# Performance work log

Measured on AMD Instinct MI355X. Metric: run time of the kernel, lower is better.

Reference implementation:

```python
import jax, jax.numpy as jnp
import numpy as np
import math

EMBED_DIM = 512
NUM_HEADS = 8
BLOCK_SIZE = 16
RANK = 32
B, N = 1, 4096
HEAD_DIM = EMBED_DIM // NUM_HEADS
SCALE = math.sqrt(HEAD_DIM)  # note: the torch module MULTIPLIES q by sqrt(head_dim)


def _block_causal_mask(n, block):
    # block-diagonal lower-triangular mask, identical for every head
    idx = jnp.arange(n)
    same_block = (idx[:, None] // block) == (idx[None, :] // block)
    causal = idx[:, None] >= idx[None, :]
    return (same_block & causal).astype(jnp.float32)  # [N, N]


def setup_inputs() -> dict:
    key = jax.random.key(0)
    ks = jax.random.split(key, 12)
    s = 0.02
    C, R = EMBED_DIM, RANK
    return {
        "x": jax.random.normal(ks[0], (B, N, C), dtype=jnp.float32),
        # low-rank query proj: Linear(C->R) then Linear(R->C); torch weight is [out, in]
        "q_w1": jax.random.normal(ks[1], (R, C), dtype=jnp.float32) * s,
        "q_w2": jax.random.normal(ks[2], (C, R), dtype=jnp.float32) * s,
        # key_value: Linear(C->2R) then Linear(2R->2C)
        "kv_w1": jax.random.normal(ks[3], (2 * R, C), dtype=jnp.float32) * s,
        "kv_w2": jax.random.normal(ks[4], (2 * C, 2 * R), dtype=jnp.float32) * s,
        # dynamic_focus: depthwise 1x1 conv (per-channel scale+bias) then pointwise 1x1 conv
        "dw_w": jax.random.normal(ks[5], (C,), dtype=jnp.float32) * s,
        "dw_b": jax.random.normal(ks[6], (C,), dtype=jnp.float32) * s,
        "pw_w": jax.random.normal(ks[7], (C, C), dtype=jnp.float32) * s,
        "pw_b": jax.random.normal(ks[8], (C,), dtype=jnp.float32) * s,
        # output proj: Linear(C->R) then Linear(R->C)
        "p_w1": jax.random.normal(ks[9], (R, C), dtype=jnp.float32) * s,
        "p_w2": jax.random.normal(ks[10], (C, R), dtype=jnp.float32) * s,
    }


def reference(x, q_w1, q_w2, kv_w1, kv_w2, dw_w, dw_b, pw_w, pw_b, p_w1, p_w2):
    Bv, Nv, C = x.shape
    H, D = NUM_HEADS, HEAD_DIM

    # low-rank q / kv projections (no bias)
    q = (x @ q_w1.T) @ q_w2.T                              # [B, N, C]
    kv = (x @ kv_w1.T) @ kv_w2.T                           # [B, N, 2C]

    q = q.reshape(Bv, Nv, H, D).transpose(0, 2, 1, 3)      # [B, H, N, D]
    kv = kv.reshape(Bv, Nv, 2, H, D).transpose(2, 0, 3, 1, 4)
    k, v = kv[0], kv[1]                                    # [B, H, N, D]

    q = q * SCALE
    attn = jnp.einsum("bhnd,bhmd->bhnm", q, k)             # [B, H, N, N]
    # faithful to source: full-row softmax FIRST, then block-diag causal mask
    mask = _block_causal_mask(Nv, BLOCK_SIZE)              # [N, N]
    attn = jax.nn.softmax(attn, axis=-1) * mask

    wv = jnp.einsum("bhnm,bhmd->bhnd", attn, v)            # [B, H, N, D]
    wv = wv.transpose(0, 2, 1, 3).reshape(Bv, Nv, C)       # [B, N, C]

    # dynamic_focus: depthwise 1x1 conv == per-channel affine; pointwise 1x1 conv == linear.
    # Spatial reshape to (sqrt(N), sqrt(N)) is a no-op for 1x1 convs, so stay in [B, N, C].
    dyn = wv * dw_w + dw_b
    dyn = dyn @ pw_w.T + pw_b

    y = dyn + x
    y = (y @ p_w1.T) @ p_w2.T
    return y
```

## Files before the change

kernel.cpp:

```cpp
#include <hip/hip_runtime.h>

#define NFULL 4096
#define CDIM  512
#define HEADS 8
#define DDIM  64

typedef unsigned short u16;
typedef short bf16x8 __attribute__((ext_vector_type(8)));
typedef float f32x4 __attribute__((ext_vector_type(4)));

#if __has_builtin(__builtin_amdgcn_exp2f)
__device__ __forceinline__ float exp2_hw(float x) { return __builtin_amdgcn_exp2f(x); }
#else
__device__ __forceinline__ float exp2_hw(float x) {
  float r;
  asm volatile("v_exp_f32 %0, %1\n\ts_nop 1" : "=v"(r) : "v"(x));
  return r;
}
#endif
#define EXP2(x) exp2_hw(x)

#define QSCALE 11.541560327111707f

__device__ __forceinline__ float dot4(float4 a, float4 b) {
  return a.x * b.x + a.y * b.y + a.z * b.z + a.w * b.w;
}

__device__ __forceinline__ u16 f2bf(float x) {
  union { float f; unsigned u; } v; v.f = x;
  unsigned r = v.u + 0x7fffu + ((v.u >> 16) & 1u);
  return (u16)(r >> 16);
}

__global__ __launch_bounds__(256) void k_pre(const float* __restrict__ x,
                                             const float* __restrict__ qw1,
                                             const float* __restrict__ kvw1,
                                             float* __restrict__ t_part,
                                             const float* __restrict__ pww,
                                             const float* __restrict__ dww,
                                             const float* __restrict__ dwb,
                                             const float* __restrict__ pwb,
                                             float* __restrict__ bias2,
                                             u16* __restrict__ pwbf) {
  __shared__ __align__(16) u16 Xs[64][72];
  __shared__ __align__(16) u16 Ws[96][72];
  const int tid = threadIdx.x;
  if (blockIdx.x >= 128) {
    const int b = blockIdx.x - 128;
    if (b < 2) {
      const int c = b * 256 + tid;
      float acc = 0.f;
      for (int e = 0; e < 512; e += 4)
        acc += dot4(*(const float4*)&pww[(size_t)c * 512 + e], *(const float4*)&dwb[e]);
      bias2[c] = acc + pwb[c];
    } else {
      const int base = (b - 2) * 4096 + tid * 16;
      const int e0 = base & 511;
      u16 o[16];
#pragma unroll
      for (int q = 0; q < 4; ++q) {
        const float4 w = *(const float4*)&pww[base + q * 4];
        const float4 d = *(const float4*)&dww[e0 + q * 4];
        o[q * 4 + 0] = f2bf(w.x * d.x); o[q * 4 + 1] = f2bf(w.y * d.y);
        o[q * 4 + 2] = f2bf(w.z * d.z); o[q * 4 + 3] = f2bf(w.w * d.w);
      }
      *(uint4*)&pwbf[base] = *(const uint4*)&o[0];
      *(uint4*)&pwbf[base + 8] = *(const uint4*)&o[8];
    }
    return;
  }

  const int rb = blockIdx.x >> 1, ks = blockIdx.x & 1;
  const int r0 = rb * 64;
  const int wave = tid >> 6, lane = tid & 63;
  const int lrow = lane & 15, g = lane >> 4;

  f32x4 acc[6];
#pragma unroll
  for (int sub = 0; sub < 6; ++sub) acc[sub] = (f32x4){0.f, 0.f, 0.f, 0.f};

  for (int k0 = ks * 256; k0 < ks * 256 + 256; k0 += 64) {
    __syncthreads();
    {
      const int row = tid >> 2, c16 = (tid & 3) * 16;
      const float* __restrict__ src = x + (size_t)(r0 + row) * 512 + k0 + c16;
      u16 tmp[16];
#pragma unroll
      for (int q = 0; q < 4; ++q) {
        const float4 v = *(const float4*)(src + q * 4);
        tmp[q * 4 + 0] = f2bf(v.x); tmp[q * 4 + 1] = f2bf(v.y);
        tmp[q * 4 + 2] = f2bf(v.z); tmp[q * 4 + 3] = f2bf(v.w);
      }
      *(uint4*)&Xs[row][c16] = *(const uint4*)&tmp[0];
      *(uint4*)&Xs[row][c16 + 8] = *(const uint4*)&tmp[8];
    }
    for (int u = tid; u < 384; u += 256) {
      const int c = u >> 2, c16 = (u & 3) * 16;
      const float* __restrict__ src =
          (c < 32 ? qw1 + (size_t)c * 512 : kvw1 + (size_t)(c - 32) * 512) + k0 + c16;
      u16 tmp[16];
#pragma unroll
      for (int q = 0; q < 4; ++q) {
        const float4 v = *(const float4*)(src + q * 4);
        tmp[q * 4 + 0] = f2bf(v.x); tmp[q * 4 + 1] = f2bf(v.y);
        tmp[q * 4 + 2] = f2bf(v.z); tmp[q * 4 + 3] = f2bf(v.w);
      }
      *(uint4*)&Ws[c][c16] = *(const uint4*)&tmp[0];
      *(uint4*)&Ws[c][c16 + 8] = *(const uint4*)&tmp[8];
    }
    __syncthreads();
    const bf16x8 a0 = *(const bf16x8*)&Xs[wave * 16 + lrow][g * 8];
    const bf16x8 a1 = *(const bf16x8*)&Xs[wave * 16 + lrow][32 + g * 8];
#pragma unroll
    for (int sub = 0; sub < 6; ++sub) {
      const bf16x8 b0 = *(const bf16x8*)&Ws[sub * 16 + lrow][g * 8];
      const bf16x8 b1 = *(const bf16x8*)&Ws[sub * 16 + lrow][32 + g * 8];
      acc[sub] = __builtin_amdgcn_mfma_f32_16x16x32_bf16(a0, b0, acc[sub], 0, 0, 0);
      acc[sub] = __builtin_amdgcn_mfma_f32_16x16x32_bf16(a1, b1, acc[sub], 0, 0, 0);
    }
  }
  float* __restrict__ tp = t_part + (size_t)ks * NFULL * 96;
#pragma unroll
  for (int sub = 0; sub < 6; ++sub)
#pragma unroll
    for (int j = 0; j < 4; ++j)
      tp[(size_t)(r0 + wave * 16 + g * 4 + j) * 96 + sub * 16 + lrow] = acc[sub][j];
}

__global__ __launch_bounds__(256) void k_proj2(const float* __restrict__ t_part,
                                               const float* __restrict__ qw2,
                                               const float* __restrict__ kvw2,
                                               u16* __restrict__ qb,
                                               u16* __restrict__ kb,
                                               float* __restrict__ vh) {
  __shared__ __align__(16) u16 Ts[64][72];
  __shared__ __align__(16) u16 Wsh[128][72];
  const int cb = blockIdx.x % 12;
  const int r0 = (blockIdx.x / 12) * 64;
  const int tid = threadIdx.x;
  const int wave = tid >> 6, lane = tid & 63;
  const int lrow = lane & 15, g = lane >> 4;
  const bool isq = cb < 4;
  const int c0 = isq ? cb * 128 : 512 + (cb - 4) * 128;
  const float* __restrict__ tp0 = t_part;
  const float* __restrict__ tp1 = t_part + (size_t)NFULL * 96;

  if (isq) {
    for (int u = tid; u < 512; u += 256) {
      const int row = u >> 3, c4 = (u & 7) * 4;
      const size_t gi = (size_t)(r0 + row) * 96 + c4;
      const float4 p0 = *(const float4*)&tp0[gi];
      const float4 p1 = *(const float4*)&tp1[gi];
      u16 tmp[4] = {f2bf(p0.x + p1.x), f2bf(p0.y + p1.y),
                    f2bf(p0.z + p1.z), f2bf(p0.w + p1.w)};
      *(uint2*)&Ts[row][c4] = *(const uint2*)&tmp[0];
    }
  } else {
    for (int u = tid; u < 1024; u += 256) {
      const int row = u >> 4, c4 = (u & 15) * 4;
      const size_t gi = (size_t)(r0 + row) * 96 + 32 + c4;
      const float4 p0 = *(const float4*)&tp0[gi];
      const float4 p1 = *(const float4*)&tp1[gi];
      u16 tmp[4] = {f2bf(p0.x + p1.x), f2bf(p0.y + p1.y),
                    f2bf(p0.z + p1.z), f2bf(p0.w + p1.w)};
      *(uint2*)&Ts[row][c4] = *(const uint2*)&tmp[0];
    }
  }
  if (isq) {
    for (int u = tid; u < 1024; u += 256) {
      const int col = u >> 3, cf = (u & 7) * 4;
      const float4 v = *(const float4*)&qw2[(size_t)(c0 + col) * 32 + cf];
      u16 tmp[4] = {f2bf(v.x), f2bf(v.y), f2bf(v.z), f2bf(v.w)};
      *(uint2*)&Wsh[col][cf] = *(const uint2*)&tmp[0];
    }
  } else {
    for (int u = tid; u < 2048; u += 256) {
      const int col = u >> 4, cf = (u & 15) * 4;
      const float4 v = *(const float4*)&kvw2[(size_t)(c0 - 512 + col) * 64 + cf];
      u16 tmp[4] = {f2bf(v.x), f2bf(v.y), f2bf(v.z), f2bf(v.w)};
      *(uint2*)&Wsh[col][cf] = *(const uint2*)&tmp[0];
    }
  }
  __syncthreads();

  if (isq) {
    const bf16x8 aq = *(const bf16x8*)&Ts[wave * 16 + lrow][g * 8];
#pragma unroll
    for (int sub = 0; sub < 8; ++sub) {
      const bf16x8 b0 = *(const bf16x8*)&Wsh[sub * 16 + lrow][g * 8];
      f32x4 acc = {0.f, 0.f, 0.f, 0.f};
      acc = __builtin_amdgcn_mfma_f32_16x16x32_bf16(aq, b0, acc, 0, 0, 0);
      const int colg = c0 + sub * 16 + lrow;
#pragma unroll
      for (int j = 0; j < 4; ++j) {
        const int n = r0 + wave * 16 + g * 4 + j;
        qb[((size_t)(colg >> 6) * NFULL + n) * 64 + (colg & 63)] = f2bf(acc[j] * QSCALE);
      }
    }
  } else {
    const bf16x8 a0 = *(const bf16x8*)&Ts[wave * 16 + lrow][g * 8];
    const bf16x8 a1 = *(const bf16x8*)&Ts[wave * 16 + lrow][32 + g * 8];
#pragma unroll
    for (int sub = 0; sub < 8; ++sub) {
      const bf16x8 b0 = *(const bf16x8*)&Wsh[sub * 16 + lrow][g * 8];
      const bf16x8 b1 = *(const bf16x8*)&Wsh[sub * 16 + lrow][32 + g * 8];
      f32x4 acc = {0.f, 0.f, 0.f, 0.f};
      acc = __builtin_amdgcn_mfma_f32_16x16x32_bf16(a0, b0, acc, 0, 0, 0);
      acc = __builtin_amdgcn_mfma_f32_16x16x32_bf16(a1, b1, acc, 0, 0, 0);
      const int colg = c0 + sub * 16 + lrow;
#pragma unroll
      for (int j = 0; j < 4; ++j) {
        const int n = r0 + wave * 16 + g * 4 + j;
        if (colg < 1024) {
          const int c2 = colg - 512;
          kb[((size_t)(c2 >> 6) * NFULL + n) * 64 + (c2 & 63)] = f2bf(acc[j]);
        } else {
          const int c2 = colg - 1024;
          vh[((size_t)(c2 >> 6) * NFULL + n) * 64 + (c2 & 63)] = acc[j];
        }
      }
    }
  }
}

__global__ __launch_bounds__(256, 4) void k_attn(const u16* __restrict__ qb,
                                                 const u16* __restrict__ kb,
                                                 const float* __restrict__ vh,
                                                 float* __restrict__ wv,
                                                 float* __restrict__ dsp) {
  __shared__ __align__(16) u16 KB[4][64][64];
  __shared__ float P_lds[4][16][17];
  __shared__ float Ds[4][4][16];

  const int h = blockIdx.x & 7;
  const int qt = (blockIdx.x >> 3) & 63;
  const int s = blockIdx.x >> 9;
  const int q0 = qt * 64;
  const int tid = threadIdx.x;
  const int wave = tid >> 6, lane = tid & 63;
  const int lrow = lane & 15, g = lane >> 4;

  const u16* __restrict__ Qg = qb + ((size_t)h * NFULL + q0) * 64;
  const u16* __restrict__ Kg = kb + ((size_t)h * NFULL + (size_t)s * 2048) * 64;

  bf16x8 qf[4][2];
#pragma unroll
  for (int f = 0; f < 4; ++f) {
    qf[f][0] = *(const bf16x8*)&Qg[(f * 16 + lrow) * 64 + g * 8];
    qf[f][1] = *(const bf16x8*)&Qg[(f * 16 + lrow) * 64 + 32 + g * 8];
  }

  const int srow8 = lane >> 3;
  const int scol = ((lane & 7) ^ srow8) << 3;

#define STAGE(T, B)                                                           \
  do {                                                                        \
    const u16* tb_ = Kg + (size_t)(T) * 64 * 64;                              \
    {                                                                         \
      const u16* src_ = tb_ + (wave * 16 + srow8) * 64 + scol;                \
      u16* dst_ = &KB[(B)][wave * 16][0];                                     \
      __builtin_amdgcn_global_load_lds(                                       \
          (const __attribute__((address_space(1))) unsigned*)src_,            \
          (__attribute__((address_space(3))) unsigned*)dst_, 16, 0, 0);       \
    }                                                                         \
    {                                                                         \
      const u16* src_ = tb_ + (wave * 16 + 8 + srow8) * 64 + scol;            \
      u16* dst_ = &KB[(B)][wave * 16][0] + 512;                               \
      __builtin_amdgcn_global_load_lds(                                       \
          (const __attribute__((address_space(1))) unsigned*)src_,            \
          (__attribute__((address_space(3))) unsigned*)dst_, 16, 0, 0);       \
    }                                                                         \
  } while (0)

  const int rsw = wave * 16 + lrow;
  const int x0 = (g ^ (lrow & 7)) * 8;
  const int x1 = ((g + 4) ^ (lrow & 7)) * 8;

  float dsum[4] = {0.f, 0.f, 0.f, 0.f};
  const bool dg = (s == (qt >> 5));
  const int tdiag = qt & 31;

  auto tile = [&](int t, int b) {
    const bf16x8 kf0 = *(const bf16x8*)&KB[b][rsw][x0];
    const bf16x8 kf1 = *(const bf16x8*)&KB[b][rsw][x1];
    f32x4 a[4];
    __builtin_amdgcn_s_setprio(1);
#pragma unroll
    for (int f = 0; f < 4; ++f) {
      f32x4 t4 = {0.f, 0.f, 0.f, 0.f};
      t4 = __builtin_amdgcn_mfma_f32_16x16x32_bf16(kf0, qf[f][0], t4, 0, 0, 0);
      t4 = __builtin_amdgcn_mfma_f32_16x16x32_bf16(kf1, qf[f][1], t4, 0, 0, 0);
      a[f] = t4;
    }
    __builtin_amdgcn_s_setprio(0);
    const bool isd = dg && (t == tdiag);
#pragma unroll
    for (int f = 0; f < 4; ++f) {
      const float e0 = EXP2(a[f][0]);
      const float e1 = EXP2(a[f][1]);
      const float e2 = EXP2(a[f][2]);
      const float e3 = EXP2(a[f][3]);
      dsum[f] += (e0 + e1) + (e2 + e3);
      if (isd && f == wave) {
        const int rr = g * 4;
        P_lds[wave][rr + 0][lrow] = (rr + 0 <= lrow) ? e0 : 0.f;
        P_lds[wave][rr + 1][lrow] = (rr + 1 <= lrow) ? e1 : 0.f;
        P_lds[wave][rr + 2][lrow] = (rr + 2 <= lrow) ? e2 : 0.f;
        P_lds[wave][rr + 3][lrow] = (rr + 3 <= lrow) ? e3 : 0.f;
      }
    }
  };

  STAGE(0, 0); STAGE(1, 1); STAGE(2, 2);

  for (int t = 0; t < 28; t += 2) {
    STAGE(t + 3, (t + 3) & 3);
    asm volatile("s_waitcnt vmcnt(6)" ::: "memory");
    tile(t, t & 3);
    STAGE(t + 4, (t + 4) & 3);
    asm volatile("s_waitcnt vmcnt(6)" ::: "memory");
    tile(t + 1, (t + 1) & 3);
  }
  STAGE(31, 3);
  asm volatile("s_waitcnt vmcnt(6)" ::: "memory");
  tile(28, 0);
  asm volatile("s_waitcnt vmcnt(4)" ::: "memory");
  tile(29, 1);
  asm volatile("s_waitcnt vmcnt(2)" ::: "memory");
  tile(30, 2);
  asm volatile("s_waitcnt vmcnt(0)" ::: "memory");
  tile(31, 3);
#undef STAGE

#pragma unroll
  for (int f = 0; f < 4; ++f) {
    dsum[f] += __shfl_xor(dsum[f], 16);
    dsum[f] += __shfl_xor(dsum[f], 32);
  }
  if (g == 0) {
#pragma unroll
    for (int f = 0; f < 4; ++f) Ds[wave][f][lrow] = dsum[f];
  }
  __syncthreads();

  if (tid < 64) {
    const int f = tid >> 4, r = tid & 15;
    const float den = Ds[0][f][r] + Ds[1][f][r] + Ds[2][f][r] + Ds[3][f][r];
    dsp[((size_t)s * HEADS + h) * NFULL + q0 + f * 16 + r] = den;
  }

  if (dg) {
    const float* __restrict__ V =
        vh + ((size_t)h * NFULL + q0 + wave * 16) * 64 + g * 16;
    float o[16];
#pragma unroll
    for (int dd = 0; dd < 16; ++dd) o[dd] = 0.f;
#pragma unroll
    for (int k = 0; k < 16; ++k) {
      const float p = P_lds[wave][k][lrow];
      const float4 v0 = *(const float4*)&V[k * 64 + 0];
      const float4 v1 = *(const float4*)&V[k * 64 + 4];
      const float4 v2 = *(const float4*)&V[k * 64 + 8];
      const float4 v3 = *(const float4*)&V[k * 64 + 12];
      o[0] += p * v0.x;  o[1] += p * v0.y;  o[2] += p * v0.z;  o[3] += p * v0.w;
      o[4] += p * v1.x;  o[5] += p * v1.y;  o[6] += p * v1.z;  o[7] += p * v1.w;
      o[8] += p * v2.x;  o[9] += p * v2.y;  o[10] += p * v2.z; o[11] += p * v2.w;
      o[12] += p * v3.x; o[13] += p * v3.y; o[14] += p * v3.z; o[15] += p * v3.w;
    }
    float* __restrict__ op =
        wv + (size_t)(q0 + wave * 16 + lrow) * CDIM + h * 64 + g * 16;
#pragma unroll
    for (int c4 = 0; c4 < 4; ++c4) {
      float4 r;
      r.x = o[c4 * 4 + 0]; r.y = o[c4 * 4 + 1];
      r.z = o[c4 * 4 + 2]; r.w = o[c4 * 4 + 3];
      *(float4*)&op[c4 * 4] = r;
    }
  }
}

__global__ __launch_bounds__(256) void k_dyn(const float* __restrict__ wv,
                                             const float* __restrict__ x,
                                             const u16* __restrict__ pwbf,
                                             const float* __restrict__ bias2,
                                             const float* __restrict__ dsp,
                                             u16* __restrict__ y16) {
  __shared__ __align__(16) u16 Ab[64][72];
  __shared__ __align__(16) u16 Wb[64][72];
  const int rb = blockIdx.x >> 3, cb = blockIdx.x & 7;
  const int r0 = rb * 64, c0 = cb * 64;
  const int tid = threadIdx.x;
  const int wave = tid >> 6, lane = tid & 63;
  const int lrow = lane & 15, g = lane >> 4;
  const int srow = tid >> 2;
  const int skc = (tid & 3) * 16;

  float inv8[8];
#pragma unroll
  for (int hh = 0; hh < 8; ++hh) {
    const size_t base = (size_t)hh * NFULL + r0 + srow;
    inv8[hh] = 1.0f / (dsp[base] + dsp[(size_t)8 * NFULL + base]);
  }

  f32x4 acc[4];
#pragma unroll
  for (int ct = 0; ct < 4; ++ct) acc[ct] = (f32x4){0.f, 0.f, 0.f, 0.f};

  const float* __restrict__ ap = wv + (size_t)(r0 + srow) * 512 + skc;
  const u16* __restrict__ wp = pwbf + (size_t)(c0 + srow) * 512 + skc;
  float4 a4[4];
#pragma unroll
  for (int e = 0; e < 4; ++e) a4[e] = *(const float4*)(ap + e * 4);
  uint4 w0 = *(const uint4*)wp;
  uint4 w1 = *(const uint4*)(wp + 8);

  for (int k0 = 0; k0 < 512; k0 += 64) {
    const float sc = inv8[k0 >> 6];
    u16 ab16[16];
#pragma unroll
    for (int e = 0; e < 4; ++e) {
      ab16[e * 4 + 0] = f2bf(a4[e].x * sc);
      ab16[e * 4 + 1] = f2bf(a4[e].y * sc);
      ab16[e * 4 + 2] = f2bf(a4[e].z * sc);
      ab16[e * 4 + 3] = f2bf(a4[e].w * sc);
    }
    __syncthreads();
    *(uint4*)&Ab[srow][skc] = *(const uint4*)&ab16[0];
    *(uint4*)&Ab[srow][skc + 8] = *(const uint4*)&ab16[8];
    *(uint4*)&Wb[srow][skc] = w0;
    *(uint4*)&Wb[srow][skc + 8] = w1;
    __syncthreads();
    if (k0 + 64 < 512) {
#pragma unroll
      for (int e = 0; e < 4; ++e) a4[e] = *(const float4*)(ap + k0 + 64 + e * 4);
      w0 = *(const uint4*)(wp + k0 + 64);
      w1 = *(const uint4*)(wp + k0 + 64 + 8);
    }
#pragma unroll
    for (int kk = 0; kk < 2; ++kk) {
      const bf16x8 af = *(const bf16x8*)&Ab[wave * 16 + lrow][kk * 32 + g * 8];
#pragma unroll
      for (int ct = 0; ct < 4; ++ct) {
        const bf16x8 wf = *(const bf16x8*)&Wb[ct * 16 + lrow][kk * 32 + g * 8];
        acc[ct] = __builtin_amdgcn_mfma_f32_16x16x32_bf16(wf, af, acc[ct], 0, 0, 0);
      }
    }
  }
  const int row = r0 + wave * 16 + lrow;
#pragma unroll
  for (int ct = 0; ct < 4; ++ct) {
    const int c = c0 + ct * 16 + g * 4;
    const float4 bb = *(const float4*)&bias2[c];
    const float4 xv = *(const float4*)&x[(size_t)row * 512 + c];
    u16 o4[4];
    o4[0] = f2bf(acc[ct][0] + bb.x + xv.x);
    o4[1] = f2bf(acc[ct][1] + bb.y + xv.y);
    o4[2] = f2bf(acc[ct][2] + bb.z + xv.z);
    o4[3] = f2bf(acc[ct][3] + bb.w + xv.w);
    *(uint2*)&y16[(size_t)row * 512 + c] = *(const uint2*)o4;
  }
}

__global__ __launch_bounds__(256) void k_pout(const u16* __restrict__ y16,
                                              const float* __restrict__ pw1,
                                              const float* __restrict__ pw2,
                                              float* __restrict__ out) {
  __shared__ __align__(16) u16 yb[16][520];
  __shared__ float tp_part[2][32][17];
  const int r0 = blockIdx.x * 16;
  const int tid = threadIdx.x;
  const int wave = tid >> 6, lane = tid & 63;
  const int lrow = lane & 15, g = lane >> 4;

  for (int rep = 0; rep < 4; ++rep) {
    const int idx = rep * 256 + tid;
    const int row = idx >> 6, c8 = (idx & 63) * 8;
    *(uint4*)&yb[row][c8] = *(const uint4*)&y16[(size_t)(r0 + row) * 512 + c8];
  }
  __syncthreads();

  {
    const int ct1 = wave & 1, kh = wave >> 1;
    f32x4 acc = {0.f, 0.f, 0.f, 0.f};
#pragma unroll
    for (int ks = 0; ks < 8; ++ks) {
      const int K = kh * 256 + ks * 32 + g * 8;
      union { u16 a[8]; bf16x8 v; } aw;
      const float4 wv0 = *(const float4*)&pw1[(size_t)(ct1 * 16 + lrow) * 512 + K];
      const float4 wv1 = *(const float4*)&pw1[(size_t)(ct1 * 16 + lrow) * 512 + K + 4];
      aw.a[0] = f2bf(wv0.x); aw.a[1] = f2bf(wv0.y);
      aw.a[2] = f2bf(wv0.z); aw.a[3] = f2bf(wv0.w);
      aw.a[4] = f2bf(wv1.x); aw.a[5] = f2bf(wv1.y);
      aw.a[6] = f2bf(wv1.z); aw.a[7] = f2bf(wv1.w);
      const bf16x8 bf = *(const bf16x8*)&yb[lrow][K];
      acc = __builtin_amdgcn_mfma_f32_16x16x32_bf16(aw.v, bf, acc, 0, 0, 0);
    }
#pragma unroll
    for (int j = 0; j < 4; ++j)
      tp_part[kh][ct1 * 16 + g * 4 + j][lrow] = acc[j];
  }
  __syncthreads();

  union { u16 a[8]; bf16x8 v; } bq;
#pragma unroll
  for (int i = 0; i < 8; ++i) {
    const int k = g * 8 + i;
    bq.a[i] = f2bf(tp_part[0][k][lrow] + tp_part[1][k][lrow]);
  }

#pragma unroll
  for (int t = 0; t < 8; ++t) {
    const int ct = wave * 8 + t;
    union { u16 a[8]; bf16x8 v; } aw;
    const float4 wv0 = *(const float4*)&pw2[(size_t)(ct * 16 + lrow) * 32 + g * 8];
    const float4 wv1 = *(const float4*)&pw2[(size_t)(ct * 16 + lrow) * 32 + g * 8 + 4];
    aw.a[0] = f2bf(wv0.x); aw.a[1] = f2bf(wv0.y);
    aw.a[2] = f2bf(wv0.z); aw.a[3] = f2bf(wv0.w);
    aw.a[4] = f2bf(wv1.x); aw.a[5] = f2bf(wv1.y);
    aw.a[6] = f2bf(wv1.z); aw.a[7] = f2bf(wv1.w);
    f32x4 acc = {0.f, 0.f, 0.f, 0.f};
    acc = __builtin_amdgcn_mfma_f32_16x16x32_bf16(aw.v, bq.v, acc, 0, 0, 0);
    float4 res;
    res.x = acc[0]; res.y = acc[1]; res.z = acc[2]; res.w = acc[3];
    *(float4*)&out[(size_t)(r0 + lrow) * 512 + ct * 16 + g * 4] = res;
  }
}

extern "C" void kernel_launch(void* const* d_in, const int* in_sizes, int n_in,
                              void* d_out, int out_size, void* d_ws, size_t ws_size,
                              hipStream_t stream) {
  const float* x     = (const float*)d_in[0];
  const float* q_w1  = (const float*)d_in[1];
  const float* q_w2  = (const float*)d_in[2];
  const float* kv_w1 = (const float*)d_in[3];
  const float* kv_w2 = (const float*)d_in[4];
  const float* dw_w  = (const float*)d_in[5];
  const float* dw_b  = (const float*)d_in[6];
  const float* pw_w  = (const float*)d_in[7];
  const float* pw_b  = (const float*)d_in[8];
  const float* p_w1  = (const float*)d_in[9];
  const float* p_w2  = (const float*)d_in[10];
  float* out = (float*)d_out;

  char* ws = (char*)d_ws;
  float* dsp   = (float*)ws;
  float* bias2 = (float*)(ws + 786432);
  u16*   pwbf  = (u16*)(ws + 786432 + 4096);
  u16*   qbw   = pwbf + 262144;
  u16*   kbw   = qbw + (size_t)HEADS * NFULL * DDIM;
  u16*   y16   = qbw;
  float* vh    = (float*)(kbw + (size_t)HEADS * NFULL * DDIM);
  float* wvf   = vh + (size_t)HEADS * NFULL * DDIM;
  float* t_part = wvf + (size_t)NFULL * CDIM;

  k_pre<<<194, 256, 0, stream>>>(x, q_w1, kv_w1, t_part, pw_w, dw_w, dw_b, pw_b,
                                 bias2, pwbf);
  k_proj2<<<(NFULL / 64) * 12, 256, 0, stream>>>(t_part, q_w2, kv_w2, qbw, kbw, vh);
  k_attn<<<2 * HEADS * (NFULL / 64), 256, 0, stream>>>(qbw, kbw, vh, wvf, dsp);
  k_dyn<<<(NFULL / 64) * 8, 256, 0, stream>>>(wvf, x, pwbf, bias2, dsp, y16);
  k_pout<<<NFULL / 16, 256, 0, stream>>>(y16, p_w1, p_w2, out);
}
```

Measured before the change: 89.35 us.

## Store intermediates in bf16, drop split-K partials, pre-convert output proj weights

The first projection stops splitting K across two blocks. Each block now handles 32 rows over the full K and writes the rank-96 intermediate directly as bf16, so k_proj2 no longer sums two fp32 partials. The attention output is stored as bf16 instead of fp32, halving that tensor's write and read traffic in k_dyn. The output projection weights are converted to bf16 once in k_pre rather than by every k_pout block. These changes cut global memory traffic and repeated conversion work, at the cost of an extra bf16 rounding on wv before the dsp scale is applied, and a k_pre grid of 128 row blocks with longer K loops.

```diff
diff --git a/kernel.cpp b/kernel.cpp
--- a/kernel.cpp
+++ b/kernel.cpp
@@ -32,19 +32,29 @@
   return (u16)(r >> 16);
 }
 
+__device__ __forceinline__ float bf2f(u16 b) {
+  union { unsigned u; float f; } v; v.u = ((unsigned)b) << 16;
+  return v.f;
+}
+
 __global__ __launch_bounds__(256) void k_pre(const float* __restrict__ x,
                                              const float* __restrict__ qw1,
                                              const float* __restrict__ kvw1,
-                                             float* __restrict__ t_part,
+                                             u16* __restrict__ t_bf,
                                              const float* __restrict__ pww,
                                              const float* __restrict__ dww,
                                              const float* __restrict__ dwb,
                                              const float* __restrict__ pwb,
+                                             const float* __restrict__ pw1,
+                                             const float* __restrict__ pw2,
                                              float* __restrict__ bias2,
-                                             u16* __restrict__ pwbf) {
-  __shared__ __align__(16) u16 Xs[64][72];
+                                             u16* __restrict__ pwbf,
+                                             u16* __restrict__ pw1bf,
+                                             u16* __restrict__ pw2bf) {
+  __shared__ __align__(16) u16 Xs[32][72];
   __shared__ __align__(16) u16 Ws[96][72];
   const int tid = threadIdx.x;
+
   if (blockIdx.x >= 128) {
     const int b = blockIdx.x - 128;
     if (b < 2) {
@@ -54,80 +64,82 @@
         acc += dot4(*(const float4*)&pww[(size_t)c * 512 + e], *(const float4*)&dwb[e]);
       bias2[c] = acc + pwb[c];
     } else {
-      const int base = (b - 2) * 4096 + tid * 16;
+      const float* src;
+      u16* dst;
+      bool scale = false;
+      int base;
+      if (b < 66)      { base = (b - 2) * 4096 + tid * 16;  src = pww; dst = pwbf; scale = true; }
+      else if (b < 70) { base = (b - 66) * 4096 + tid * 16; src = pw1; dst = pw1bf; }
+      else             { base = (b - 70) * 4096 + tid * 16; src = pw2; dst = pw2bf; }
       const int e0 = base & 511;
       u16 o[16];
 #pragma unroll
       for (int q = 0; q < 4; ++q) {
-        const float4 w = *(const float4*)&pww[base + q * 4];
-        const float4 d = *(const float4*)&dww[e0 + q * 4];
-        o[q * 4 + 0] = f2bf(w.x * d.x); o[q * 4 + 1] = f2bf(w.y * d.y);
-        o[q * 4 + 2] = f2bf(w.z * d.z); o[q * 4 + 3] = f2bf(w.w * d.w);
+        float4 w = *(const float4*)&src[base + q * 4];
+        if (scale) {
+          const float4 d = *(const float4*)&dww[e0 + q * 4];
+          w.x *= d.x; w.y *= d.y; w.z *= d.z; w.w *= d.w;
+        }
+        o[q * 4 + 0] = f2bf(w.x); o[q * 4 + 1] = f2bf(w.y);
+        o[q * 4 + 2] = f2bf(w.z); o[q * 4 + 3] = f2bf(w.w);
       }
-      *(uint4*)&pwbf[base] = *(const uint4*)&o[0];
-      *(uint4*)&pwbf[base + 8] = *(const uint4*)&o[8];
+      *(uint4*)&dst[base] = *(const uint4*)&o[0];
+      *(uint4*)&dst[base + 8] = *(const uint4*)&o[8];
     }
     return;
   }
 
-  const int rb = blockIdx.x >> 1, ks = blockIdx.x & 1;
-  const int r0 = rb * 64;
+  const int r0 = blockIdx.x * 32;
   const int wave = tid >> 6, lane = tid & 63;
   const int lrow = lane & 15, g = lane >> 4;
-
-  f32x4 acc[6];
-#pragma unroll
-  for (int sub = 0; sub < 6; ++sub) acc[sub] = (f32x4){0.f, 0.f, 0.f, 0.f};
-
-  for (int k0 = ks * 256; k0 < ks * 256 + 256; k0 += 64) {
+  const int rs = wave >> 1, ws2 = wave & 1;
+
+  f32x4 acc[3];
+#pragma unroll
+  for (int sub = 0; sub < 3; ++sub) acc[sub] = (f32x4){0.f, 0.f, 0.f, 0.f};
+
+  for (int k0 = 0; k0 < 512; k0 += 64) {
     __syncthreads();
     {
-      const int row = tid >> 2, c16 = (tid & 3) * 16;
+      const int row = tid >> 3, c16 = (tid & 7) * 8;
       const float* __restrict__ src = x + (size_t)(r0 + row) * 512 + k0 + c16;
-      u16 tmp[16];
-#pragma unroll
-      for (int q = 0; q < 4; ++q) {
-        const float4 v = *(const float4*)(src + q * 4);
-        tmp[q * 4 + 0] = f2bf(v.x); tmp[q * 4 + 1] = f2bf(v.y);
-        tmp[q * 4 + 2] = f2bf(v.z); tmp[q * 4 + 3] = f2bf(v.w);
-      }
+      const float4 v0 = *(const float4*)(src);
+      const float4 v1 = *(const float4*)(src + 4);
+      u16 tmp[8] = {f2bf(v0.x), f2bf(v0.y), f2bf(v0.z), f2bf(v0.w),
+                    f2bf(v1.x), f2bf(v1.y), f2bf(v1.z), f2bf(v1.w)};
       *(uint4*)&Xs[row][c16] = *(const uint4*)&tmp[0];
-      *(uint4*)&Xs[row][c16 + 8] = *(const uint4*)&tmp[8];
-    }
-    for (int u = tid; u < 384; u += 256) {
-      const int c = u >> 2, c16 = (u & 3) * 16;
+    }
+    for (int u = tid; u < 768; u += 256) {
+      const int c = u >> 3, c16 = (u & 7) * 8;
       const float* __restrict__ src =
           (c < 32 ? qw1 + (size_t)c * 512 : kvw1 + (size_t)(c - 32) * 512) + k0 + c16;
-      u16 tmp[16];
-#pragma unroll
-      for (int q = 0; q < 4; ++q) {
-        const float4 v = *(const float4*)(src + q * 4);
-        tmp[q * 4 + 0] = f2bf(v.x); tmp[q * 4 + 1] = f2bf(v.y);
-        tmp[q * 4 + 2] = f2bf(v.z); tmp[q * 4 + 3] = f2bf(v.w);
-      }
+      const float4 v0 = *(const float4*)(src);
+      const float4 v1 = *(const float4*)(src + 4);
+      u16 tmp[8] = {f2bf(v0.x), f2bf(v0.y), f2bf(v0.z), f2bf(v0.w),
+                    f2bf(v1.x), f2bf(v1.y), f2bf(v1.z), f2bf(v1.w)};
       *(uint4*)&Ws[c][c16] = *(const uint4*)&tmp[0];
-      *(uint4*)&Ws[c][c16 + 8] = *(const uint4*)&tmp[8];
     }
     __syncthreads();
-    const bf16x8 a0 = *(const bf16x8*)&Xs[wave * 16 + lrow][g * 8];
-    const bf16x8 a1 = *(const bf16x8*)&Xs[wave * 16 + lrow][32 + g * 8];
-#pragma unroll
-    for (int sub = 0; sub < 6; ++sub) {
-      const bf16x8 b0 = *(const bf16x8*)&Ws[sub * 16 + lrow][g * 8];
-      const bf16x8 b1 = *(const bf16x8*)&Ws[sub * 16 + lrow][32 + g * 8];
+    const bf16x8 a0 = *(const bf16x8*)&Xs[rs * 16 + lrow][g * 8];
+    const bf16x8 a1 = *(const bf16x8*)&Xs[rs * 16 + lrow][32 + g * 8];
+#pragma unroll
+    for (int sub = 0; sub < 3; ++sub) {
+      const int c = (ws2 * 3 + sub) * 16 + lrow;
+      const bf16x8 b0 = *(const bf16x8*)&Ws[c][g * 8];
+      const bf16x8 b1 = *(const bf16x8*)&Ws[c][32 + g * 8];
       acc[sub] = __builtin_amdgcn_mfma_f32_16x16x32_bf16(a0, b0, acc[sub], 0, 0, 0);
       acc[sub] = __builtin_amdgcn_mfma_f32_16x16x32_bf16(a1, b1, acc[sub], 0, 0, 0);
     }
   }
-  float* __restrict__ tp = t_part + (size_t)ks * NFULL * 96;
-#pragma unroll
-  for (int sub = 0; sub < 6; ++sub)
+#pragma unroll
+  for (int sub = 0; sub < 3; ++sub)
 #pragma unroll
     for (int j = 0; j < 4; ++j)
-      tp[(size_t)(r0 + wave * 16 + g * 4 + j) * 96 + sub * 16 + lrow] = acc[sub][j];
-}
-
-__global__ __launch_bounds__(256) void k_proj2(const float* __restrict__ t_part,
+      t_bf[(size_t)(r0 + rs * 16 + g * 4 + j) * 96 + (ws2 * 3 + sub) * 16 + lrow] =
+          f2bf(acc[sub][j]);
+}
+
+__global__ __launch_bounds__(256) void k_proj2(const u16* __restrict__ t_bf,
                                                const float* __restrict__ qw2,
                                                const float* __restrict__ kvw2,
                                                u16* __restrict__ qb,
@@ -142,29 +154,16 @@
   const int lrow = lane & 15, g = lane >> 4;
   const bool isq = cb < 4;
   const int c0 = isq ? cb * 128 : 512 + (cb - 4) * 128;
-  const float* __restrict__ tp0 = t_part;
-  const float* __restrict__ tp1 = t_part + (size_t)NFULL * 96;
-
-  if (isq) {
-    for (int u = tid; u < 512; u += 256) {
-      const int row = u >> 3, c4 = (u & 7) * 4;
-      const size_t gi = (size_t)(r0 + row) * 96 + c4;
-      const float4 p0 = *(const float4*)&tp0[gi];
-      const float4 p1 = *(const float4*)&tp1[gi];
-      u16 tmp[4] = {f2bf(p0.x + p1.x), f2bf(p0.y + p1.y),
-                    f2bf(p0.z + p1.z), f2bf(p0.w + p1.w)};
-      *(uint2*)&Ts[row][c4] = *(const uint2*)&tmp[0];
-    }
-  } else {
-    for (int u = tid; u < 1024; u += 256) {
-      const int row = u >> 4, c4 = (u & 15) * 4;
-      const size_t gi = (size_t)(r0 + row) * 96 + 32 + c4;
-      const float4 p0 = *(const float4*)&tp0[gi];
-      const float4 p1 = *(const float4*)&tp1[gi];
-      u16 tmp[4] = {f2bf(p0.x + p1.x), f2bf(p0.y + p1.y),
-                    f2bf(p0.z + p1.z), f2bf(p0.w + p1.w)};
-      *(uint2*)&Ts[row][c4] = *(const uint2*)&tmp[0];
-    }
+
+  for (int u = tid; u < 512; u += 256) {
+    const int row = u >> 3, ch = (u & 7) * 8;
+    uint4 v = {0u, 0u, 0u, 0u};
+    if (isq) {
+      if (ch < 32) v = *(const uint4*)&t_bf[(size_t)(r0 + row) * 96 + ch];
+    } else {
+      v = *(const uint4*)&t_bf[(size_t)(r0 + row) * 96 + 32 + ch];
+    }
+    *(uint4*)&Ts[row][ch] = v;
   }
   if (isq) {
     for (int u = tid; u < 1024; u += 256) {
@@ -226,7 +225,7 @@
 __global__ __launch_bounds__(256, 4) void k_attn(const u16* __restrict__ qb,
                                                  const u16* __restrict__ kb,
                                                  const float* __restrict__ vh,
-                                                 float* __restrict__ wv,
+                                                 u16* __restrict__ wv16,
                                                  float* __restrict__ dsp) {
   __shared__ __align__(16) u16 KB[4][64][64];
   __shared__ float P_lds[4][16][17];
@@ -367,19 +366,17 @@
       o[8] += p * v2.x;  o[9] += p * v2.y;  o[10] += p * v2.z; o[11] += p * v2.w;
       o[12] += p * v3.x; o[13] += p * v3.y; o[14] += p * v3.z; o[15] += p * v3.w;
     }
-    float* __restrict__ op =
-        wv + (size_t)(q0 + wave * 16 + lrow) * CDIM + h * 64 + g * 16;
-#pragma unroll
-    for (int c4 = 0; c4 < 4; ++c4) {
-      float4 r;
-      r.x = o[c4 * 4 + 0]; r.y = o[c4 * 4 + 1];
-      r.z = o[c4 * 4 + 2]; r.w = o[c4 * 4 + 3];
-      *(float4*)&op[c4 * 4] = r;
-    }
-  }
-}
-
-__global__ __launch_bounds__(256) void k_dyn(const float* __restrict__ wv,
+    u16 ob[16];
+#pragma unroll
+    for (int dd = 0; dd < 16; ++dd) ob[dd] = f2bf(o[dd]);
+    u16* __restrict__ op =
+        wv16 + (size_t)(q0 + wave * 16 + lrow) * CDIM + h * 64 + g * 16;
+    *(uint4*)&op[0] = *(const uint4*)&ob[0];
+    *(uint4*)&op[8] = *(const uint4*)&ob[8];
+  }
+}
+
+__global__ __launch_bounds__(256) void k_dyn(const u16* __restrict__ wv16,
                                              const float* __restrict__ x,
                                              const u16* __restrict__ pwbf,
                                              const float* __restrict__ bias2,
@@ -406,24 +403,22 @@
 #pragma unroll
   for (int ct = 0; ct < 4; ++ct) acc[ct] = (f32x4){0.f, 0.f, 0.f, 0.f};
 
-  const float* __restrict__ ap = wv + (size_t)(r0 + srow) * 512 + skc;
+  const u16* __restrict__ ap = wv16 + (size_t)(r0 + srow) * 512 + skc;
   const u16* __restrict__ wp = pwbf + (size_t)(c0 + srow) * 512 + skc;
-  float4 a4[4];
-#pragma unroll
-  for (int e = 0; e < 4; ++e) a4[e] = *(const float4*)(ap + e * 4);
+  uint4 av0 = *(const uint4*)ap;
+  uint4 av1 = *(const uint4*)(ap + 8);
   uint4 w0 = *(const uint4*)wp;
   uint4 w1 = *(const uint4*)(wp + 8);
 
   for (int k0 = 0; k0 < 512; k0 += 64) {
     const float sc = inv8[k0 >> 6];
     u16 ab16[16];
-#pragma unroll
-    for (int e = 0; e < 4; ++e) {
-      ab16[e * 4 + 0] = f2bf(a4[e].x * sc);
-      ab16[e * 4 + 1] = f2bf(a4[e].y * sc);
-      ab16[e * 4 + 2] = f2bf(a4[e].z * sc);
-      ab16[e * 4 + 3] = f2bf(a4[e].w * sc);
-    }
+    const u16* pa0 = (const u16*)&av0;
+    const u16* pa1 = (const u16*)&av1;
+#pragma unroll
+    for (int e = 0; e < 8; ++e) ab16[e] = f2bf(bf2f(pa0[e]) * sc);
+#pragma unroll
+    for (int e = 0; e < 8; ++e) ab16[8 + e] = f2bf(bf2f(pa1[e]) * sc);
     __syncthreads();
     *(uint4*)&Ab[srow][skc] = *(const uint4*)&ab16[0];
     *(uint4*)&Ab[srow][skc + 8] = *(const uint4*)&ab16[8];
@@ -431,8 +426,8 @@
     *(uint4*)&Wb[srow][skc + 8] = w1;
     __syncthreads();
     if (k0 + 64 < 512) {
-#pragma unroll
-      for (int e = 0; e < 4; ++e) a4[e] = *(const float4*)(ap + k0 + 64 + e * 4);
+      av0 = *(const uint4*)(ap + k0 + 64);
+      av1 = *(const uint4*)(ap + k0 + 64 + 8);
       w0 = *(const uint4*)(wp + k0 + 64);
       w1 = *(const uint4*)(wp + k0 + 64 + 8);
     }
@@ -462,8 +457,8 @@
 }
 
 __global__ __launch_bounds__(256) void k_pout(const u16* __restrict__ y16,
-                                              const float* __restrict__ pw1,
-                                              const float* __restrict__ pw2,
+                                              const u16* __restrict__ pw1bf,
+                                              const u16* __restrict__ pw2bf,
                                               float* __restrict__ out) {
   __shared__ __align__(16) u16 yb[16][520];
   __shared__ float tp_part[2][32][17];
@@ -485,15 +480,9 @@
 #pragma unroll
     for (int ks = 0; ks < 8; ++ks) {
       const int K = kh * 256 + ks * 32 + g * 8;
-      union { u16 a[8]; bf16x8 v; } aw;
-      const float4 wv0 = *(const float4*)&pw1[(size_t)(ct1 * 16 + lrow) * 512 + K];
-      const float4 wv1 = *(const float4*)&pw1[(size_t)(ct1 * 16 + lrow) * 512 + K + 4];
-      aw.a[0] = f2bf(wv0.x); aw.a[1] = f2bf(wv0.y);
-      aw.a[2] = f2bf(wv0.z); aw.a[3] = f2bf(wv0.w);
-      aw.a[4] = f2bf(wv1.x); aw.a[5] = f2bf(wv1.y);
-      aw.a[6] = f2bf(wv1.z); aw.a[7] = f2bf(wv1.w);
+      const bf16x8 aw = *(const bf16x8*)&pw1bf[(size_t)(ct1 * 16 + lrow) * 512 + K];
       const bf16x8 bf = *(const bf16x8*)&yb[lrow][K];
-      acc = __builtin_amdgcn_mfma_f32_16x16x32_bf16(aw.v, bf, acc, 0, 0, 0);
+      acc = __builtin_amdgcn_mfma_f32_16x16x32_bf16(aw, bf, acc, 0, 0, 0);
     }
 #pragma unroll
     for (int j = 0; j < 4; ++j)
@@ -511,15 +500,9 @@
 #pragma unroll
   for (int t = 0; t < 8; ++t) {
     const int ct = wave * 8 + t;
-    union { u16 a[8]; bf16x8 v; } aw;
-    const float4 wv0 = *(const float4*)&pw2[(size_t)(ct * 16 + lrow) * 32 + g * 8];
-    const float4 wv1 = *(const float4*)&pw2[(size_t)(ct * 16 + lrow) * 32 + g * 8 + 4];
-    aw.a[0] = f2bf(wv0.x); aw.a[1] = f2bf(wv0.y);
-    aw.a[2] = f2bf(wv0.z); aw.a[3] = f2bf(wv0.w);
-    aw.a[4] = f2bf(wv1.x); aw.a[5] = f2bf(wv1.y);
-    aw.a[6] = f2bf(wv1.z); aw.a[7] = f2bf(wv1.w);
+    const bf16x8 aw = *(const bf16x8*)&pw2bf[(size_t)(ct * 16 + lrow) * 32 + g * 8];
     f32x4 acc = {0.f, 0.f, 0.f, 0.f};
-    acc = __builtin_amdgcn_mfma_f32_16x16x32_bf16(aw.v, bq.v, acc, 0, 0, 0);
+    acc = __builtin_amdgcn_mfma_f32_16x16x32_bf16(aw, bq.v, acc, 0, 0, 0);
     float4 res;
     res.x = acc[0]; res.y = acc[1]; res.z = acc[2]; res.w = acc[3];
     *(float4*)&out[(size_t)(r0 + lrow) * 512 + ct * 16 + g * 4] = res;
@@ -544,19 +527,21 @@
 
   char* ws = (char*)d_ws;
   float* dsp   = (float*)ws;
-  float* bias2 = (float*)(ws + 786432);
-  u16*   pwbf  = (u16*)(ws + 786432 + 4096);
-  u16*   qbw   = pwbf + 262144;
+  float* bias2 = (float*)(ws + 262144);
+  u16*   pwbf  = (u16*)(ws + 262144 + 4096);
+  u16*   pw1bf = pwbf + 262144;
+  u16*   pw2bf = pw1bf + 16384;
+  u16*   t_bf  = pw2bf + 16384;
+  u16*   qbw   = t_bf + (size_t)NFULL * 96;
   u16*   kbw   = qbw + (size_t)HEADS * NFULL * DDIM;
+  float* vh    = (float*)(kbw + (size_t)HEADS * NFULL * DDIM);
+  u16*   wv16  = (u16*)(vh + (size_t)HEADS * NFULL * DDIM);
   u16*   y16   = qbw;
-  float* vh    = (float*)(kbw + (size_t)HEADS * NFULL * DDIM);
-  float* wvf   = vh + (size_t)HEADS * NFULL * DDIM;
-  float* t_part = wvf + (size_t)NFULL * CDIM;
-
-  k_pre<<<194, 256, 0, stream>>>(x, q_w1, kv_w1, t_part, pw_w, dw_w, dw_b, pw_b,
-                                 bias2, pwbf);
-  k_proj2<<<(NFULL / 64) * 12, 256, 0, stream>>>(t_part, q_w2, kv_w2, qbw, kbw, vh);
-  k_attn<<<2 * HEADS * (NFULL / 64), 256, 0, stream>>>(qbw, kbw, vh, wvf, dsp);
-  k_dyn<<<(NFULL / 64) * 8, 256, 0, stream>>>(wvf, x, pwbf, bias2, dsp, y16);
-  k_pout<<<NFULL / 16, 256, 0, stream>>>(y16, p_w1, p_w2, out);
-}
+
+  k_pre<<<202, 256, 0, stream>>>(x, q_w1, kv_w1, t_bf, pw_w, dw_w, dw_b, pw_b,
+                                 p_w1, p_w2, bias2, pwbf, pw1bf, pw2bf);
+  k_proj2<<<(NFULL / 64) * 12, 256, 0, stream>>>(t_bf, q_w2, kv_w2, qbw, kbw, vh);
+  k_attn<<<2 * HEADS * (NFULL / 64), 256, 0, stream>>>(qbw, kbw, vh, wv16, dsp);
+  k_dyn<<<(NFULL / 64) * 8, 256, 0, stream>>>(wv16, x, pwbf, bias2, dsp, y16);
+  k_pout<<<NFULL / 16, 256, 0, stream>>>(y16, pw1bf, pw2bf, out);
+}
```

Result: faster. 83.33 us (-6.7%).
